# Kernel optimization log

Measured on AMD Instinct MI355X. Metric: run time of the kernel, lower is better.

Reference implementation:

```python
import jax, jax.numpy as jnp
import numpy as np

BEV_H, BEV_W, ED, HEADS, HD, LEVELS, POINTS, LAYERS = 200, 200, 128, 8, 16, 4, 8, 2
SPATIAL = [(128, 256), (64, 128), (32, 64), (16, 32)]
NV = sum(h * w for h, w in SPATIAL)
NQ = BEV_H * BEV_W
NCLS = 21


def setup_inputs() -> dict:
    key = jax.random.key(0)
    ks = iter(jax.random.split(key, 48))
    r = lambda shape, s=0.02: jax.random.normal(next(ks), shape, jnp.float32) * s
    inp = dict(
        value=r((1, NV, ED), 1.0),
        bev_queries=r((NQ, ED), 0.02),
        bev_pos=r((NQ, ED), 0.02),
        proj_indices=jax.random.randint(next(ks), (1, BEV_H, BEV_W), 0, 250000),
        Wv=r((LAYERS, ED, ED)), bv=jnp.zeros((LAYERS, ED)),
        Woff=r((LAYERS, ED, HEADS * LEVELS * POINTS * 2), 0.01),
        boff=jnp.zeros((LAYERS, HEADS * LEVELS * POINTS * 2)),
        Wattn=r((LAYERS, ED, HEADS * LEVELS * POINTS), 0.01),
        battn=jnp.zeros((LAYERS, HEADS * LEVELS * POINTS)),
        Wout=r((LAYERS, ED, ED)), bout=jnp.zeros((LAYERS, ED)),
        Wf1=r((LAYERS, ED, ED)), bf1=jnp.zeros((LAYERS, ED)),
        Wf2=r((LAYERS, ED, ED)), bf2=jnp.zeros((LAYERS, ED)),
        ln_g=jnp.ones((LAYERS, 2, ED)), ln_b=jnp.zeros((LAYERS, 2, ED)),
        cw1=r((128, ED, 7, 7), 0.01), g1=jnp.ones(128), b1=jnp.zeros(128),
        cw2=r((64, 128, 3, 3), 0.02), g2=jnp.ones(64), b2=jnp.zeros(64),
        cw3=r((48, 64, 3, 3), 0.02), g3=jnp.ones(48), b3=jnp.zeros(48),
        cw4=r((48, 48, 3, 3), 0.02), g4=jnp.ones(48), b4=jnp.zeros(48),
        objw=r((NCLS, 48, 1, 1), 0.05), objb=jnp.zeros(NCLS),
    )
    return inp


def _ln(x, g, b):
    m = x.mean(-1, keepdims=True)
    v = ((x - m) ** 2).mean(-1, keepdims=True)
    return (x - m) * jax.lax.rsqrt(v + 1e-5) * g + b


def _deform_attn(q, value, Wv, bv, Woff, boff, Wattn, battn, Wout, bout, ref):
    # multi-scale deformable attention (Deformable-DETR / BEVFormer core)
    v = (value[0] @ Wv + bv).reshape(NV, HEADS, HD)
    off = (q @ Woff + boff).reshape(NQ, HEADS, LEVELS, POINTS, 2)
    attn = jax.nn.softmax((q @ Wattn + battn).reshape(NQ, HEADS, LEVELS * POINTS), -1)
    attn = attn.reshape(NQ, HEADS, LEVELS, POINTS)
    out = jnp.zeros((HEADS, NQ, HD), jnp.float32)
    start = 0
    for l, (H, W) in enumerate(SPATIAL):
        vl = v[start:start + H * W].transpose(1, 0, 2)  # [HEADS, H*W, HD]
        start += H * W
        # normalized sampling locations in [0,1]
        loc = ref[:, None, None, :] + off[:, :, l] / jnp.array([W, H], jnp.float32)
        x = loc[..., 0] * W - 0.5  # grid_sample align_corners=False convention
        y = loc[..., 1] * H - 0.5  # [NQ, HEADS, POINTS]
        x0 = jnp.floor(x)
        y0 = jnp.floor(y)
        acc = jnp.zeros((HEADS, NQ, POINTS, HD), jnp.float32)
        for dx, dy in ((0, 0), (1, 0), (0, 1), (1, 1)):
            xc = x0 + dx
            yc = y0 + dy
            wgt = (1.0 - jnp.abs(x - xc)) * (1.0 - jnp.abs(y - yc))
            valid = (xc >= 0) & (xc < W) & (yc >= 0) & (yc < H)
            xi = jnp.clip(xc, 0, W - 1).astype(jnp.int32)
            yi = jnp.clip(yc, 0, H - 1).astype(jnp.int32)
            idx = (yi * W + xi).transpose(1, 0, 2)  # [HEADS, NQ, POINTS]
            g = jax.vmap(lambda vh, ih: vh[ih])(vl, idx)  # [HEADS, NQ, POINTS, HD]
            acc = acc + (wgt * valid).transpose(1, 0, 2)[..., None] * g
        out = out + jnp.einsum('nhp,hnpd->hnd', attn[:, :, l], acc)
    return out.transpose(1, 0, 2).reshape(NQ, ED) @ Wout + bout


def _bev_encoder(bev_queries, bev_pos, value, Wv, bv, Woff, boff, Wattn, battn, Wout, bout, Wf1, bf1, Wf2, bf2, ln_g, ln_b):
    gx = (jnp.arange(BEV_W, dtype=jnp.float32) + 0.5) / BEV_W
    gy = (jnp.arange(BEV_H, dtype=jnp.float32) + 0.5) / BEV_H
    ref = jnp.stack(jnp.meshgrid(gx, gy), -1).reshape(NQ, 2)  # (x, y)
    q = bev_queries
    for i in range(LAYERS):  # operation_order: cross_attn, norm, ffn, norm
        a = _deform_attn(q + bev_pos, value, Wv[i], bv[i], Woff[i], boff[i],
                         Wattn[i], battn[i], Wout[i], bout[i], ref)
        q = _ln(q + a, ln_g[i, 0], ln_b[i, 0])
        h = jax.nn.relu(q @ Wf1[i] + bf1[i]) @ Wf2[i] + bf2[i]
        q = _ln(q + h, ln_g[i, 1], ln_b[i, 1])
    return q


def _conv(x, w, p):
    return jax.lax.conv_general_dilated(x, w, (1, 1), [(p, p), (p, p)],
                                        dimension_numbers=('NCHW', 'OIHW', 'NCHW'))


def _bn_relu(x, g, b):
    m = x.mean((0, 2, 3), keepdims=True)
    v = x.var((0, 2, 3), keepdims=True)
    return jax.nn.relu((x - m) * jax.lax.rsqrt(v + 1e-5) * g[None, :, None, None] + b[None, :, None, None])


def reference(value, bev_queries, bev_pos, proj_indices, Wv, bv, Woff, boff, Wattn, battn, Wout, bout, Wf1, bf1, Wf2, bf2, ln_g, ln_b, cw1, g1, b1, cw2, g2, b2, cw3, g3, b3, cw4, g4, b4, objw, objb):
    observed_masks = proj_indices < jnp.max(proj_indices)  # mask_update
    q = _bev_encoder(bev_queries, bev_pos, value, Wv, bv, Woff, boff, Wattn, battn,
                     Wout, bout, Wf1, bf1, Wf2, bf2, ln_g, ln_b)
    mem = q.reshape(1, BEV_H, BEV_W, ED).transpose(0, 3, 1, 2)  # [1, ED, H, W]
    h = _bn_relu(_conv(mem, cw1, 3), g1, b1)
    h = _bn_relu(_conv(h, cw2, 1), g2, b2)
    h = _bn_relu(_conv(h, cw3, 1), g3, b3)
    h = _bn_relu(_conv(h, cw4, 1), g4, b4)
    semmap = _conv(h, objw, 0) + objb[None, :, None, None]
    return semmap, observed_masks
```

## Files before the change

kernel.cpp:

```cpp
#include <hip/hip_runtime.h>
#include <cstdint>
#include <cstddef>

#define NQ 40000
#define EDIM 128
#define NVAL 43520
#define NCLS 21

typedef unsigned short u16;
typedef unsigned int uint;
typedef short bf16x8 __attribute__((ext_vector_type(8)));
typedef float f32x4 __attribute__((ext_vector_type(4)));

__device__ inline u16 f2b(float f) {
    unsigned u = __float_as_uint(f);
    unsigned r = u + 0x7FFF + ((u >> 16) & 1);
    return (u16)(r >> 16);
}
__device__ inline float b2f(u16 v) {
    unsigned u = ((unsigned)v) << 16;
    return __uint_as_float(u);
}
__device__ inline float blo(uint u) { return __uint_as_float(u << 16); }
__device__ inline float bhi(uint u) { return __uint_as_float(u & 0xFFFF0000u); }

__global__ void reduce_max_int(const int* __restrict__ idx, int* __restrict__ mx) {
    int i = blockIdx.x * 256 + threadIdx.x;
    int v = (i < NQ) ? idx[i] : 0;
    for (int o = 32; o > 0; o >>= 1) v = max(v, __shfl_xor(v, o, 64));
    if ((threadIdx.x & 63) == 0) atomicMax(mx, v);
}

__global__ void write_mask(const int* __restrict__ idx, const int* __restrict__ mx,
                           float* __restrict__ out) {
    int i = blockIdx.x * 256 + threadIdx.x;
    if (i >= NQ) return;
    out[i] = (idx[i] < *mx) ? 1.0f : 0.0f;
}

__global__ void cvt_b_k(const float* __restrict__ src, u16* __restrict__ dst, int n8) {
    int i = blockIdx.x * 256 + threadIdx.x;
    if (i >= n8) return;
    const float4 a = ((const float4*)src)[i * 2];
    const float4 b = ((const float4*)src)[i * 2 + 1];
    u16 o[8] = {f2b(a.x), f2b(a.y), f2b(a.z), f2b(a.w), f2b(b.x), f2b(b.y), f2b(b.z), f2b(b.w)};
    ((uint4*)dst)[i] = *(const uint4*)o;
}

__global__ void add2b_k(const float* __restrict__ a, const float* __restrict__ b,
                        u16* __restrict__ c, int n8) {
    int i = blockIdx.x * 256 + threadIdx.x;
    if (i >= n8) return;
    const float4 a0 = ((const float4*)a)[i * 2], a1 = ((const float4*)a)[i * 2 + 1];
    const float4 b0 = ((const float4*)b)[i * 2], b1 = ((const float4*)b)[i * 2 + 1];
    u16 o[8] = {f2b(a0.x + b0.x), f2b(a0.y + b0.y), f2b(a0.z + b0.z), f2b(a0.w + b0.w),
                f2b(a1.x + b1.x), f2b(a1.y + b1.y), f2b(a1.z + b1.z), f2b(a1.w + b1.w)};
    ((uint4*)c)[i] = *(const uint4*)o;
}

__global__ void pack_enc_k(const float* __restrict__ Wv, const float* __restrict__ Woff,
                           const float* __restrict__ Wattn, const float* __restrict__ Wout,
                           const float* __restrict__ Wf1, const float* __restrict__ Wf2,
                           u16* __restrict__ dst) {
    int i = blockIdx.x * 256 + threadIdx.x;
    if (i >= 327680) return;
    int l = i / 163840, r = i % 163840;
    int k = r / 1280, col = r % 1280;
    const float* src; int N; int n; u16* d;
    u16* base = dst + (size_t)l * 163840;
    if (col < 128)       { src = Wv    + (size_t)l * 16384; N = 128; n = col;        d = base;          }
    else if (col < 640)  { src = Woff  + (size_t)l * 65536; N = 512; n = col - 128;  d = base + 16384;  }
    else if (col < 896)  { src = Wattn + (size_t)l * 32768; N = 256; n = col - 640;  d = base + 81920;  }
    else if (col < 1024) { src = Wout  + (size_t)l * 16384; N = 128; n = col - 896;  d = base + 114688; }
    else if (col < 1152) { src = Wf1   + (size_t)l * 16384; N = 128; n = col - 1024; d = base + 131072; }
    else                 { src = Wf2   + (size_t)l * 16384; N = 128; n = col - 1152; d = base + 147456; }
    d[(size_t)n * 128 + k] = f2b(src[(size_t)k * N + n]);
}

__global__ void pack_bias_k(const float* __restrict__ boff, const float* __restrict__ battn,
                            float* __restrict__ dst) {
    int i = blockIdx.x * 256 + threadIdx.x;
    if (i >= 1536) return;
    int l = i / 768, r = i % 768;
    dst[i] = (r < 512) ? boff[(size_t)l * 512 + r] : battn[(size_t)l * 256 + r - 512];
}

__global__ void pack_cw_k(const float* __restrict__ w, u16* __restrict__ wT,
                          int OC, int IC, int KS, int OCp, int ICp) {
    int i = blockIdx.x * 256 + threadIdx.x;
    int tot = KS * KS * OCp * ICp;
    if (i >= tot) return;
    int ic = i % ICp; int r = i / ICp;
    int oc = r % OCp; int tap = r / OCp;
    int ky = tap / KS, kx = tap % KS;
    float v = 0.f;
    if (oc < OC && ic < IC)
        v = w[(((size_t)oc * IC + ic) * KS + ky) * KS + kx];
    wT[i] = f2b(v);
}

__global__ __launch_bounds__(256) void gemm_mfma_k(
        const u16* __restrict__ A, const u16* __restrict__ BT,
        const float* __restrict__ bias, float* __restrict__ Cf,
        u16* __restrict__ Cb, int N, int relu) {
    __shared__ u16 As[64 * 136];
    __shared__ u16 Bs[64 * 136];
    const int m0 = blockIdx.x * 64, n0 = blockIdx.y * 64;
    const int t = threadIdx.x;
#pragma unroll
    for (int ci = t; ci < 1024; ci += 256) {
        int r = ci >> 4, c = ci & 15;
        *(uint4*)&As[r * 136 + c * 8] = *(const uint4*)&A[(size_t)(m0 + r) * 128 + c * 8];
        *(uint4*)&Bs[r * 136 + c * 8] = *(const uint4*)&BT[(size_t)(n0 + r) * 128 + c * 8];
    }
    __syncthreads();
    const int wave = t >> 6, lane = t & 63;
    const int wm = (wave & 1) * 32, wn = (wave >> 1) * 32;
    const int lr = lane & 15, lk = (lane >> 4) * 8;
    f32x4 acc[2][2] = {};
#pragma unroll
    for (int ks = 0; ks < 4; ks++) {
        bf16x8 a0 = *(const bf16x8*)&As[(wm + lr) * 136 + ks * 32 + lk];
        bf16x8 a1 = *(const bf16x8*)&As[(wm + 16 + lr) * 136 + ks * 32 + lk];
        bf16x8 b0 = *(const bf16x8*)&Bs[(wn + lr) * 136 + ks * 32 + lk];
        bf16x8 b1 = *(const bf16x8*)&Bs[(wn + 16 + lr) * 136 + ks * 32 + lk];
        acc[0][0] = __builtin_amdgcn_mfma_f32_16x16x32_bf16(a0, b0, acc[0][0], 0, 0, 0);
        acc[0][1] = __builtin_amdgcn_mfma_f32_16x16x32_bf16(a0, b1, acc[0][1], 0, 0, 0);
        acc[1][0] = __builtin_amdgcn_mfma_f32_16x16x32_bf16(a1, b0, acc[1][0], 0, 0, 0);
        acc[1][1] = __builtin_amdgcn_mfma_f32_16x16x32_bf16(a1, b1, acc[1][1], 0, 0, 0);
    }
    float bj0 = bias[n0 + wn + lr];
    float bj1 = bias[n0 + wn + 16 + lr];
#pragma unroll
    for (int i = 0; i < 2; i++) {
#pragma unroll
        for (int j = 0; j < 2; j++) {
            float bb = j ? bj1 : bj0;
#pragma unroll
            for (int r = 0; r < 4; r++) {
                int ml = wm + i * 16 + (lane >> 4) * 4 + r;
                int nl = wn + j * 16 + lr;
                float v = acc[i][j][r] + bb;
                if (relu) v = fmaxf(v, 0.f);
                size_t o = (size_t)(m0 + ml) * N + n0 + nl;
                if (Cf) Cf[o] = v;
                if (Cb) Cb[o] = f2b(v);
            }
        }
    }
}

template <int KS, int ICP>
__global__ __launch_bounds__(256) void conv3_mfma_k(
        const u16* __restrict__ pimg, const u16* __restrict__ wT,
        float* __restrict__ out, int OCtot) {
    constexpr int PAD = KS / 2;
    constexpr int WIN = 64 + KS - 1;
    constexpr int LDSTR = ICP + 8;
    constexpr int KSTEPS = ICP / 32;
    constexpr int CHUNKS = 2 * WIN * (ICP / 8);
    __shared__ u16 As[2 * WIN * LDSTR];
    const int bx = blockIdx.x;
    const int y = (bx >> 2) * 2;
    const int xc = bx & 3;
    const int x0 = (xc == 3) ? 136 : xc * 64;
    const int n0 = blockIdx.y * 64;
    const int t = threadIdx.x;
    const int wave = t >> 6, lane = t & 63;
    const int rowsel = wave >> 1;
    const int wn = (wave & 1) * 32;
    const int lr = lane & 15, lkq = lane >> 4, lk = lkq * 8;
    f32x4 acc[4][2] = {};
    bf16x8 bbA[2][KSTEPS], bbB[2][KSTEPS];

    auto loadB = [&](int tap, bf16x8 (&bb)[2][KSTEPS]) {
        const u16* wb = wT + ((size_t)tap * OCtot + n0) * ICP;
#pragma unroll
        for (int ks = 0; ks < KSTEPS; ks++) {
            bb[0][ks] = *(const bf16x8*)&wb[(size_t)(wn + lr) * ICP + ks * 32 + lk];
            bb[1][ks] = *(const bf16x8*)&wb[(size_t)(wn + 16 + lr) * ICP + ks * 32 + lk];
        }
    };

    for (int ky = 0; ky < KS; ky++) {
        __syncthreads();
        for (int ci = t; ci < CHUNKS; ci += 256) {
            int w2 = ci / (WIN * (ICP / 8));
            int rem = ci - w2 * WIN * (ICP / 8);
            int r = rem / (ICP / 8), c = rem - r * (ICP / 8);
            const u16* src = pimg +
                (((size_t)(y + w2 + ky + 3 - PAD)) * 208 + (x0 + 3 - PAD)) * ICP;
            *(uint4*)&As[(w2 * WIN + r) * LDSTR + c * 8] = *(const uint4*)&src[(size_t)r * ICP + c * 8];
        }
        __syncthreads();
        loadB(ky * KS, bbA);
        const u16* asb = &As[rowsel * WIN * LDSTR];
#pragma unroll
        for (int kx = 0; kx < KS; kx++) {
            if (kx + 1 < KS) {
                if (kx & 1) loadB(ky * KS + kx + 1, bbA);
                else        loadB(ky * KS + kx + 1, bbB);
            }
#pragma unroll
            for (int ks = 0; ks < KSTEPS; ks++) {
                bf16x8 a0 = *(const bf16x8*)&asb[(lr + kx) * LDSTR + ks * 32 + lk];
                bf16x8 a1 = *(const bf16x8*)&asb[(lr + 16 + kx) * LDSTR + ks * 32 + lk];
                bf16x8 a2 = *(const bf16x8*)&asb[(lr + 32 + kx) * LDSTR + ks * 32 + lk];
                bf16x8 a3 = *(const bf16x8*)&asb[(lr + 48 + kx) * LDSTR + ks * 32 + lk];
#pragma unroll
                for (int j = 0; j < 2; j++) {
                    bf16x8 bj = (kx & 1) ? bbB[j][ks] : bbA[j][ks];
                    acc[0][j] = __builtin_amdgcn_mfma_f32_16x16x32_bf16(a0, bj, acc[0][j], 0, 0, 0);
                    acc[1][j] = __builtin_amdgcn_mfma_f32_16x16x32_bf16(a1, bj, acc[1][j], 0, 0, 0);
                    acc[2][j] = __builtin_amdgcn_mfma_f32_16x16x32_bf16(a2, bj, acc[2][j], 0, 0, 0);
                    acc[3][j] = __builtin_amdgcn_mfma_f32_16x16x32_bf16(a3, bj, acc[3][j], 0, 0, 0);
                }
            }
        }
    }
    const int px0 = (y + rowsel) * 200 + x0;
#pragma unroll
    for (int i = 0; i < 4; i++) {
#pragma unroll
        for (int j = 0; j < 2; j++) {
#pragma unroll
            for (int r = 0; r < 4; r++) {
                int ml = i * 16 + lkq * 4 + r;
                int nl = wn + j * 16 + lr;
                out[(size_t)(px0 + ml) * OCtot + n0 + nl] = acc[i][j][r];
            }
        }
    }
}

__global__ __launch_bounds__(256) void deform2_k(
        const u16* __restrict__ v, const u16* __restrict__ oa,
        u16* __restrict__ outb, int q0, int nq) {
    const int t = threadIdx.x;
    const int wq = t >> 6;
    const int lane = t & 63;
    const int h = lane >> 3;
    const int cl = lane & 7;
    const int qi = blockIdx.x * 4 + wq;
    if (qi >= nq) return;
    const int gq = q0 + qi;
    const float rx = ((gq % 200) + 0.5f) / 200.f;
    const float ry = ((gq / 200) + 0.5f) / 200.f;

    const uint* lp = (const uint*)(oa + (size_t)qi * 768 + 512 + h * 32);
    uint lw[16];
#pragma unroll
    for (int i = 0; i < 16; i++) lw[i] = lp[i];
    float lg[32];
#pragma unroll
    for (int i = 0; i < 16; i++) { lg[2 * i] = blo(lw[i]); lg[2 * i + 1] = bhi(lw[i]); }
    float mx = -1e30f;
#pragma unroll
    for (int i = 0; i < 32; i++) mx = fmaxf(mx, lg[i]);
    float ssum = 0.f;
#pragma unroll
    for (int i = 0; i < 32; i++) { lg[i] = __expf(lg[i] - mx); ssum += lg[i]; }
    const float inv = 1.f / ssum;

    const uint* op = (const uint*)(oa + (size_t)qi * 768 + h * 64);

    const int HS[4] = {128, 64, 32, 16};
    const int WS[4] = {256, 128, 64, 32};
    const int ST[4] = {0, 32768, 40960, 43008};
    float acc0 = 0.f, acc1 = 0.f;
#pragma unroll
    for (int l = 0; l < 4; l++) {
        const int H = HS[l], W = WS[l];
        const float fW = (float)W, fH = (float)H;
        const u16* vb = v + (size_t)ST[l] * 128 + h * 16 + cl * 2;
#pragma unroll
        for (int p = 0; p < 8; p++) {
            uint pr = op[l * 8 + p];
            float ox = blo(pr), oy = bhi(pr);
            float xx = rx * fW + ox - 0.5f;
            float yy = ry * fH + oy - 0.5f;
            float xf = floorf(xx), yf = floorf(yy);
            int ix = (int)xf, iy = (int)yf;
            float fx = xx - xf, fy = yy - yf;
            float aw = lg[l * 8 + p] * inv;
            int x1 = ix + 1, y1 = iy + 1;
            bool vx0 = (unsigned)ix < (unsigned)W;
            bool vx1 = (unsigned)x1 < (unsigned)W;
            bool vy0 = (unsigned)iy < (unsigned)H;
            bool vy1 = (unsigned)y1 < (unsigned)H;
            int cx0 = min(max(ix, 0), W - 1), cx1 = min(max(x1, 0), W - 1);
            int cy0 = min(max(iy, 0), H - 1), cy1 = min(max(y1, 0), H - 1);
            float w00 = (vx0 && vy0) ? (1.f - fx) * (1.f - fy) * aw : 0.f;
            float w10 = (vx1 && vy0) ? fx * (1.f - fy) * aw : 0.f;
            float w01 = (vx0 && vy1) ? (1.f - fx) * fy * aw : 0.f;
            float w11 = (vx1 && vy1) ? fx * fy * aw : 0.f;
            uint u00 = *(const uint*)(vb + (size_t)(cy0 * W + cx0) * 128);
            uint u10 = *(const uint*)(vb + (size_t)(cy0 * W + cx1) * 128);
            uint u01 = *(const uint*)(vb + (size_t)(cy1 * W + cx0) * 128);
            uint u11 = *(const uint*)(vb + (size_t)(cy1 * W + cx1) * 128);
            acc0 = fmaf(w00, blo(u00), acc0); acc1 = fmaf(w00, bhi(u00), acc1);
            acc0 = fmaf(w10, blo(u10), acc0); acc1 = fmaf(w10, bhi(u10), acc1);
            acc0 = fmaf(w01, blo(u01), acc0); acc1 = fmaf(w01, bhi(u01), acc1);
            acc0 = fmaf(w11, blo(u11), acc0); acc1 = fmaf(w11, bhi(u11), acc1);
        }
    }
    uint o = (uint)f2b(acc0) | ((uint)f2b(acc1) << 16);
    *(uint*)(outb + (size_t)gq * 128 + h * 16 + cl * 2) = o;
}

__global__ __launch_bounds__(256) void add_ln_k(
        float* __restrict__ q, const float* __restrict__ a,
        const float* __restrict__ g, const float* __restrict__ b,
        u16* __restrict__ qb) {
    const int row = blockIdx.x * 4 + (threadIdx.x >> 6);
    const int lane = threadIdx.x & 63;
    float s0 = q[(size_t)row * 128 + lane] + a[(size_t)row * 128 + lane];
    float s1 = q[(size_t)row * 128 + 64 + lane] + a[(size_t)row * 128 + 64 + lane];
    float sum = s0 + s1;
    for (int o = 32; o > 0; o >>= 1) sum += __shfl_xor(sum, o, 64);
    float mean = sum * (1.f / 128.f);
    float d0 = s0 - mean, d1 = s1 - mean;
    float vs = d0 * d0 + d1 * d1;
    for (int o = 32; o > 0; o >>= 1) vs += __shfl_xor(vs, o, 64);
    float inv = rsqrtf(vs * (1.f / 128.f) + 1e-5f);
    float o0 = d0 * inv * g[lane] + b[lane];
    float o1 = d1 * inv * g[64 + lane] + b[64 + lane];
    q[(size_t)row * 128 + lane] = o0;
    q[(size_t)row * 128 + 64 + lane] = o1;
    qb[(size_t)row * 128 + lane] = f2b(o0);
    qb[(size_t)row * 128 + 64 + lane] = f2b(o1);
}

__global__ void fill_pimg_k(const u16* __restrict__ qb, u16* __restrict__ pimg) {
    int i = blockIdx.x * 256 + threadIdx.x;
    if (i >= 640000) return;
    int p = i >> 4, c8 = i & 15;
    int y = p / 200, x = p - y * 200;
    ((uint4*)pimg)[((size_t)(y + 3) * 208 + (x + 3)) * 16 + c8] = ((const uint4*)qb)[i];
}

__global__ __launch_bounds__(256) void bn_stats2_k(const float* __restrict__ x,
                                                   float* __restrict__ acc,
                                                   int cSh, int ppb) {
    const int t = threadIdx.x;
    const int Cp = 1 << cSh;
    const int c = t & (Cp - 1);
    const int sub = t >> cSh;
    const int nsub = 256 >> cSh;
    float s = 0.f, s2 = 0.f;
    const int pbase = blockIdx.x * ppb;
    for (int i = sub; i < ppb; i += nsub) {
        float v = x[(size_t)(pbase + i) * Cp + c];
        s += v; s2 += v * v;
    }
    __shared__ float ls[256], ls2[256];
    ls[t] = s; ls2[t] = s2;
    __syncthreads();
    if (t < Cp) {
        for (int k = 1; k < nsub; k++) { s += ls[t + k * Cp]; s2 += ls2[t + k * Cp]; }
        atomicAdd(&acc[2 * t], s);
        atomicAdd(&acc[2 * t + 1], s2);
    }
}

__global__ void bn_fin_k(const float* __restrict__ acc, float* __restrict__ mv, int C) {
    int t = threadIdx.x;
    if (t >= C) return;
    float m = acc[2 * t] * (1.f / 40000.f);
    float var = acc[2 * t + 1] * (1.f / 40000.f) - m * m;
    mv[2 * t] = m;
    mv[2 * t + 1] = rsqrtf(var + 1e-5f);
}

__global__ void bn_apply_pad_k(const float* __restrict__ x, const float* __restrict__ mv,
                               const float* __restrict__ g, const float* __restrict__ b,
                               u16* __restrict__ outp, int cSh, int Creal) {
    int i = blockIdx.x * 256 + threadIdx.x;
    int Cp = 1 << cSh;
    if (i >= 40000 * Cp) return;
    int c = i & (Cp - 1);
    int p = i >> cSh;
    int y = p / 200, x_ = p - y * 200;
    float v = 0.f;
    if (c < Creal) v = fmaxf((x[i] - mv[2 * c]) * mv[2 * c + 1] * g[c] + b[c], 0.f);
    outp[((size_t)(y + 3) * 208 + (x_ + 3)) * Cp + c] = f2b(v);
}

__global__ void bn_apply2_k(const float* __restrict__ x, const float* __restrict__ mv,
                            const float* __restrict__ g, const float* __restrict__ b,
                            u16* __restrict__ outb, int cSh, int Creal) {
    int i = blockIdx.x * 256 + threadIdx.x;
    int Cp = 1 << cSh;
    if (i >= 40000 * Cp) return;
    int c = i & (Cp - 1);
    float v = 0.f;
    if (c < Creal) v = fmaxf((x[i] - mv[2 * c]) * mv[2 * c + 1] * g[c] + b[c], 0.f);
    outb[i] = f2b(v);
}

__global__ void obj_conv_k(const u16* __restrict__ in, const float* __restrict__ w,
                           const float* __restrict__ bias, float* __restrict__ out) {
    int p = blockIdx.x * 256 + threadIdx.x;
    if (p >= 40000) return;
    float xin[48];
#pragma unroll
    for (int c = 0; c < 48; c++) xin[c] = b2f(in[(size_t)p * 64 + c]);
    for (int o = 0; o < NCLS; o++) {
        float acc = bias[o];
#pragma unroll
        for (int c = 0; c < 48; c++) acc += xin[c] * w[o * 48 + c];
        out[(size_t)o * 40000 + p] = acc;
    }
}

extern "C" void kernel_launch(void* const* d_in, const int* in_sizes, int n_in,
                              void* d_out, int out_size, void* d_ws, size_t ws_size,
                              hipStream_t stream) {
    const float* value   = (const float*)d_in[0];
    const float* bev_q   = (const float*)d_in[1];
    const float* bev_pos = (const float*)d_in[2];
    const int*   proj    = (const int*)d_in[3];
    const float* Wv      = (const float*)d_in[4];
    const float* bv      = (const float*)d_in[5];
    const float* Woff    = (const float*)d_in[6];
    const float* boff    = (const float*)d_in[7];
    const float* Wattn   = (const float*)d_in[8];
    const float* battn   = (const float*)d_in[9];
    const float* Wout    = (const float*)d_in[10];
    const float* bout    = (const float*)d_in[11];
    const float* Wf1     = (const float*)d_in[12];
    const float* bf1     = (const float*)d_in[13];
    const float* Wf2     = (const float*)d_in[14];
    const float* bf2     = (const float*)d_in[15];
    const float* ln_g    = (const float*)d_in[16];
    const float* ln_b    = (const float*)d_in[17];
    const float* cw1     = (const float*)d_in[18];
    const float* g1      = (const float*)d_in[19];
    const float* b1      = (const float*)d_in[20];
    const float* cw2     = (const float*)d_in[21];
    const float* g2      = (const float*)d_in[22];
    const float* b2      = (const float*)d_in[23];
    const float* cw3     = (const float*)d_in[24];
    const float* g3      = (const float*)d_in[25];
    const float* b3      = (const float*)d_in[26];
    const float* cw4     = (const float*)d_in[27];
    const float* g4      = (const float*)d_in[28];
    const float* b4      = (const float*)d_in[29];
    const float* objw    = (const float*)d_in[30];
    const float* objb    = (const float*)d_in[31];
    float* out = (float*)d_out;

    float* WSb = (float*)d_ws;
    float* q     = WSb + 0;
    u16*   qb    = (u16*)(WSb + 5120000);
    u16*   qpb   = (u16*)(WSb + 7680000);
    u16*   valb  = (u16*)(WSb + 10240000);
    u16*   vbufb = (u16*)(WSb + 13025280);
    u16*   fb    = (u16*)(WSb + 15810560);
    float* tmp   = WSb + 18882560;
    u16*   aob   = (u16*)(WSb + 24002560);
    u16*   hb    = (u16*)(WSb + 26562560);
    u16*   wenc  = (u16*)(WSb + 29122560);
    u16*   wcv   = (u16*)(WSb + 29286400);
    float* bnacc = WSb + 29761536;
    float* bnmv  = WSb + 29762048;
    int*   maxi  = (int*)(WSb + 29762304);
    float* fbias = WSb + 29762308;

    u16*   pimg = (u16*)(WSb + 10240000);
    float* c1f  = tmp;
    u16*   c1b  = (u16*)(WSb + 13025280);
    float* c2f  = WSb + 0;
    u16*   c2b  = (u16*)(WSb + 5120000);
    float* c3f  = WSb + 2560000;
    u16*   c3b  = (u16*)(WSb + 7680000);
    float* c4f  = WSb + 0;
    u16*   c4b  = (u16*)(WSb + 15810560);

    const size_t L = 163840;
    u16* WvT[2]; u16* WoffT[2]; u16* WoutT[2]; u16* Wf1T[2]; u16* Wf2T[2];
    for (int l = 0; l < 2; l++) {
        u16* base = wenc + l * L;
        WvT[l]    = base;
        WoffT[l]  = base + 16384;
        WoutT[l]  = base + 114688;
        Wf1T[l]   = base + 131072;
        Wf2T[l]   = base + 147456;
    }
    u16* w1T = wcv;
    u16* w2T = wcv + 802816;
    u16* w3T = wcv + 876544;
    u16* w4T = wcv + 913408;

    hipMemsetAsync(maxi, 0, sizeof(int), stream);
    reduce_max_int<<<157, 256, 0, stream>>>(proj, maxi);
    write_mask<<<157, 256, 0, stream>>>(proj, maxi, out + 840000);

    pack_enc_k<<<1280, 256, 0, stream>>>(Wv, Woff, Wattn, Wout, Wf1, Wf2, wenc);
    pack_bias_k<<<6, 256, 0, stream>>>(boff, battn, fbias);
    pack_cw_k<<<3136, 256, 0, stream>>>(cw1, w1T, 128, 128, 7, 128, 128);
    pack_cw_k<<<288, 256, 0, stream>>>(cw2, w2T, 64, 128, 3, 64, 128);
    pack_cw_k<<<144, 256, 0, stream>>>(cw3, w3T, 48, 64, 3, 64, 64);
    pack_cw_k<<<144, 256, 0, stream>>>(cw4, w4T, 48, 48, 3, 64, 64);
    cvt_b_k<<<2720, 256, 0, stream>>>(value, valb, NVAL * 128 / 8);

    hipMemcpyAsync(q, bev_q, (size_t)NQ * EDIM * sizeof(float),
                   hipMemcpyDeviceToDevice, stream);
    const int CH0 = 19968, CH1 = 20032;
    for (int l = 0; l < 2; l++) {
        gemm_mfma_k<<<dim3(680, 2), 256, 0, stream>>>(
            valb, WvT[l], bv + (size_t)l * 128, nullptr, vbufb, 128, 0);
        add2b_k<<<2500, 256, 0, stream>>>(q, bev_pos, qpb, NQ * 128 / 8);
        for (int cidx = 0; cidx < 2; cidx++) {
            int qs = cidx ? CH0 : 0;
            int nq = cidx ? CH1 : CH0;
            gemm_mfma_k<<<dim3(nq / 64, 12), 256, 0, stream>>>(
                qpb + (size_t)qs * 128, WoffT[l], fbias + (size_t)l * 768,
                nullptr, fb, 768, 0);
            deform2_k<<<nq / 4, 256, 0, stream>>>(vbufb, fb, aob, qs, nq);
        }
        gemm_mfma_k<<<dim3(625, 2), 256, 0, stream>>>(
            aob, WoutT[l], bout + (size_t)l * 128, tmp, nullptr, 128, 0);
        add_ln_k<<<10000, 256, 0, stream>>>(q, tmp, ln_g + (size_t)(l * 2 + 0) * 128,
                                            ln_b + (size_t)(l * 2 + 0) * 128, qb);
        gemm_mfma_k<<<dim3(625, 2), 256, 0, stream>>>(
            qb, Wf1T[l], bf1 + (size_t)l * 128, nullptr, hb, 128, 1);
        gemm_mfma_k<<<dim3(625, 2), 256, 0, stream>>>(
            hb, Wf2T[l], bf2 + (size_t)l * 128, tmp, nullptr, 128, 0);
        add_ln_k<<<10000, 256, 0, stream>>>(q, tmp, ln_g + (size_t)(l * 2 + 1) * 128,
                                            ln_b + (size_t)(l * 2 + 1) * 128, qb);
    }

    hipMemsetAsync(pimg, 0, (size_t)206 * 208 * 128 * 2, stream);
    fill_pimg_k<<<2500, 256, 0, stream>>>(qb, pimg);

    conv3_mfma_k<7, 128><<<dim3(400, 2), 256, 0, stream>>>(pimg, w1T, c1f, 128);
    hipMemsetAsync(bnacc, 0, 512 * sizeof(float), stream);
    bn_stats2_k<<<125, 256, 0, stream>>>(c1f, bnacc, 7, 320);
    bn_fin_k<<<1, 128, 0, stream>>>(bnacc, bnmv, 128);
    hipMemsetAsync(c1b, 0, (size_t)206 * 208 * 128 * 2, stream);
    bn_apply_pad_k<<<20000, 256, 0, stream>>>(c1f, bnmv, g1, b1, c1b, 7, 128);

    conv3_mfma_k<3, 128><<<dim3(400, 1), 256, 0, stream>>>(c1b, w2T, c2f, 64);
    hipMemsetAsync(bnacc, 0, 512 * sizeof(float), stream);
    bn_stats2_k<<<125, 256, 0, stream>>>(c2f, bnacc, 6, 320);
    bn_fin_k<<<1, 64, 0, stream>>>(bnacc, bnmv, 64);
    hipMemsetAsync(c2b, 0, (size_t)206 * 208 * 64 * 2, stream);
    bn_apply_pad_k<<<10000, 256, 0, stream>>>(c2f, bnmv, g2, b2, c2b, 6, 64);

    conv3_mfma_k<3, 64><<<dim3(400, 1), 256, 0, stream>>>(c2b, w3T, c3f, 64);
    hipMemsetAsync(bnacc, 0, 512 * sizeof(float), stream);
    bn_stats2_k<<<125, 256, 0, stream>>>(c3f, bnacc, 6, 320);
    bn_fin_k<<<1, 48, 0, stream>>>(bnacc, bnmv, 48);
    hipMemsetAsync(c3b, 0, (size_t)206 * 208 * 64 * 2, stream);
    bn_apply_pad_k<<<10000, 256, 0, stream>>>(c3f, bnmv, g3, b3, c3b, 6, 48);

    conv3_mfma_k<3, 64><<<dim3(400, 1), 256, 0, stream>>>(c3b, w4T, c4f, 64);
    hipMemsetAsync(bnacc, 0, 512 * sizeof(float), stream);
    bn_stats2_k<<<125, 256, 0, stream>>>(c4f, bnacc, 6, 320);
    bn_fin_k<<<1, 48, 0, stream>>>(bnacc, bnmv, 48);
    bn_apply2_k<<<10000, 256, 0, stream>>>(c4f, bnmv, g4, b4, c4b, 6, 48);

    obj_conv_k<<<157, 256, 0, stream>>>(c4b, objw, objb, out);
}
```

Measured before the change: 1.141 ms.

## Retile conv to one row per block, widen deform loads, fuse padding into fills

The conv kernel now computes one output row per block, with a 2x2 wave split over pixels and output channels. It stages a single input row window in LDS and double-buffers the weight registers across taps, which doubles the grid and shrinks LDS use. The deformable attention kernel now handles two queries per wave and loads 4 channels per lane with 64-bit gathers. The padded image fill and the BN apply kernels write the zero border themselves, removing separate memsets. The trade-off is less reuse of weights across rows in the conv and more blocks overall.

```diff
diff --git a/kernel.cpp b/kernel.cpp
--- a/kernel.cpp
+++ b/kernel.cpp
@@ -151,81 +151,75 @@
 }
 
 template <int KS, int ICP>
-__global__ __launch_bounds__(256) void conv3_mfma_k(
+__global__ __launch_bounds__(256) void conv4_mfma_k(
         const u16* __restrict__ pimg, const u16* __restrict__ wT,
         float* __restrict__ out, int OCtot) {
     constexpr int PAD = KS / 2;
     constexpr int WIN = 64 + KS - 1;
     constexpr int LDSTR = ICP + 8;
     constexpr int KSTEPS = ICP / 32;
-    constexpr int CHUNKS = 2 * WIN * (ICP / 8);
-    __shared__ u16 As[2 * WIN * LDSTR];
+    constexpr int NTAP = KS * KS;
+    __shared__ u16 As[WIN * LDSTR];
     const int bx = blockIdx.x;
-    const int y = (bx >> 2) * 2;
+    const int y = bx >> 2;
     const int xc = bx & 3;
     const int x0 = (xc == 3) ? 136 : xc * 64;
     const int n0 = blockIdx.y * 64;
     const int t = threadIdx.x;
     const int wave = t >> 6, lane = t & 63;
-    const int rowsel = wave >> 1;
-    const int wn = (wave & 1) * 32;
+    const int wm = (wave & 1) * 32, wn = (wave >> 1) * 32;
     const int lr = lane & 15, lkq = lane >> 4, lk = lkq * 8;
-    f32x4 acc[4][2] = {};
-    bf16x8 bbA[2][KSTEPS], bbB[2][KSTEPS];
-
-    auto loadB = [&](int tap, bf16x8 (&bb)[2][KSTEPS]) {
-        const u16* wb = wT + ((size_t)tap * OCtot + n0) * ICP;
-#pragma unroll
-        for (int ks = 0; ks < KSTEPS; ks++) {
-            bb[0][ks] = *(const bf16x8*)&wb[(size_t)(wn + lr) * ICP + ks * 32 + lk];
-            bb[1][ks] = *(const bf16x8*)&wb[(size_t)(wn + 16 + lr) * ICP + ks * 32 + lk];
-        }
-    };
+
+    f32x4 acc[2][2] = {};
+    const u16* wbase = wT + (size_t)n0 * ICP;
+
+    bf16x8 cur0[KSTEPS], cur1[KSTEPS], nxt0[KSTEPS], nxt1[KSTEPS];
+#pragma unroll
+    for (int ks = 0; ks < KSTEPS; ks++) {
+        cur0[ks] = *(const bf16x8*)&wbase[(size_t)(wn + lr) * ICP + ks * 32 + lk];
+        cur1[ks] = *(const bf16x8*)&wbase[(size_t)(wn + 16 + lr) * ICP + ks * 32 + lk];
+    }
 
     for (int ky = 0; ky < KS; ky++) {
         __syncthreads();
-        for (int ci = t; ci < CHUNKS; ci += 256) {
-            int w2 = ci / (WIN * (ICP / 8));
-            int rem = ci - w2 * WIN * (ICP / 8);
-            int r = rem / (ICP / 8), c = rem - r * (ICP / 8);
-            const u16* src = pimg +
-                (((size_t)(y + w2 + ky + 3 - PAD)) * 208 + (x0 + 3 - PAD)) * ICP;
-            *(uint4*)&As[(w2 * WIN + r) * LDSTR + c * 8] = *(const uint4*)&src[(size_t)r * ICP + c * 8];
+        const u16* src = pimg + (((size_t)(y + ky + 3 - PAD)) * 208 + (x0 + 3 - PAD)) * ICP;
+        for (int ci = t; ci < WIN * (ICP / 8); ci += 256) {
+            int r = ci / (ICP / 8), c = ci - r * (ICP / 8);
+            *(uint4*)&As[r * LDSTR + c * 8] = *(const uint4*)&src[(size_t)r * ICP + c * 8];
         }
         __syncthreads();
-        loadB(ky * KS, bbA);
-        const u16* asb = &As[rowsel * WIN * LDSTR];
 #pragma unroll
         for (int kx = 0; kx < KS; kx++) {
-            if (kx + 1 < KS) {
-                if (kx & 1) loadB(ky * KS + kx + 1, bbA);
-                else        loadB(ky * KS + kx + 1, bbB);
-            }
-#pragma unroll
-            for (int ks = 0; ks < KSTEPS; ks++) {
-                bf16x8 a0 = *(const bf16x8*)&asb[(lr + kx) * LDSTR + ks * 32 + lk];
-                bf16x8 a1 = *(const bf16x8*)&asb[(lr + 16 + kx) * LDSTR + ks * 32 + lk];
-                bf16x8 a2 = *(const bf16x8*)&asb[(lr + 32 + kx) * LDSTR + ks * 32 + lk];
-                bf16x8 a3 = *(const bf16x8*)&asb[(lr + 48 + kx) * LDSTR + ks * 32 + lk];
-#pragma unroll
-                for (int j = 0; j < 2; j++) {
-                    bf16x8 bj = (kx & 1) ? bbB[j][ks] : bbA[j][ks];
-                    acc[0][j] = __builtin_amdgcn_mfma_f32_16x16x32_bf16(a0, bj, acc[0][j], 0, 0, 0);
-                    acc[1][j] = __builtin_amdgcn_mfma_f32_16x16x32_bf16(a1, bj, acc[1][j], 0, 0, 0);
-                    acc[2][j] = __builtin_amdgcn_mfma_f32_16x16x32_bf16(a2, bj, acc[2][j], 0, 0, 0);
-                    acc[3][j] = __builtin_amdgcn_mfma_f32_16x16x32_bf16(a3, bj, acc[3][j], 0, 0, 0);
+            const int tap = ky * KS + kx;
+            if (tap + 1 < NTAP) {
+                const u16* wb = wbase + (size_t)(tap + 1) * OCtot * ICP;
+#pragma unroll
+                for (int ks = 0; ks < KSTEPS; ks++) {
+                    nxt0[ks] = *(const bf16x8*)&wb[(size_t)(wn + lr) * ICP + ks * 32 + lk];
+                    nxt1[ks] = *(const bf16x8*)&wb[(size_t)(wn + 16 + lr) * ICP + ks * 32 + lk];
                 }
             }
+#pragma unroll
+            for (int ks = 0; ks < KSTEPS; ks++) {
+                bf16x8 a0 = *(const bf16x8*)&As[(wm + lr + kx) * LDSTR + ks * 32 + lk];
+                bf16x8 a1 = *(const bf16x8*)&As[(wm + 16 + lr + kx) * LDSTR + ks * 32 + lk];
+                acc[0][0] = __builtin_amdgcn_mfma_f32_16x16x32_bf16(a0, cur0[ks], acc[0][0], 0, 0, 0);
+                acc[0][1] = __builtin_amdgcn_mfma_f32_16x16x32_bf16(a0, cur1[ks], acc[0][1], 0, 0, 0);
+                acc[1][0] = __builtin_amdgcn_mfma_f32_16x16x32_bf16(a1, cur0[ks], acc[1][0], 0, 0, 0);
+                acc[1][1] = __builtin_amdgcn_mfma_f32_16x16x32_bf16(a1, cur1[ks], acc[1][1], 0, 0, 0);
+            }
+#pragma unroll
+            for (int ks = 0; ks < KSTEPS; ks++) { cur0[ks] = nxt0[ks]; cur1[ks] = nxt1[ks]; }
         }
     }
-    const int px0 = (y + rowsel) * 200 + x0;
-#pragma unroll
-    for (int i = 0; i < 4; i++) {
+    const int px0 = y * 200 + x0;
+#pragma unroll
+    for (int i = 0; i < 2; i++) {
 #pragma unroll
         for (int j = 0; j < 2; j++) {
 #pragma unroll
             for (int r = 0; r < 4; r++) {
-                int ml = i * 16 + lkq * 4 + r;
+                int ml = wm + i * 16 + lkq * 4 + r;
                 int nl = wn + j * 16 + lr;
                 out[(size_t)(px0 + ml) * OCtot + n0 + nl] = acc[i][j][r];
             }
@@ -233,27 +227,26 @@
     }
 }
 
-__global__ __launch_bounds__(256) void deform2_k(
+__global__ __launch_bounds__(256) void deform3_k(
         const u16* __restrict__ v, const u16* __restrict__ oa,
         u16* __restrict__ outb, int q0, int nq) {
     const int t = threadIdx.x;
     const int wq = t >> 6;
     const int lane = t & 63;
-    const int h = lane >> 3;
-    const int cl = lane & 7;
-    const int qi = blockIdx.x * 4 + wq;
+    const int s = lane >> 5;
+    const int l32 = lane & 31;
+    const int h = l32 >> 2;
+    const int cl = l32 & 3;
+    const int qi = blockIdx.x * 8 + wq * 2 + s;
     if (qi >= nq) return;
     const int gq = q0 + qi;
     const float rx = ((gq % 200) + 0.5f) / 200.f;
     const float ry = ((gq / 200) + 0.5f) / 200.f;
 
     const uint* lp = (const uint*)(oa + (size_t)qi * 768 + 512 + h * 32);
-    uint lw[16];
-#pragma unroll
-    for (int i = 0; i < 16; i++) lw[i] = lp[i];
     float lg[32];
 #pragma unroll
-    for (int i = 0; i < 16; i++) { lg[2 * i] = blo(lw[i]); lg[2 * i + 1] = bhi(lw[i]); }
+    for (int i = 0; i < 16; i++) { uint u = lp[i]; lg[2 * i] = blo(u); lg[2 * i + 1] = bhi(u); }
     float mx = -1e30f;
 #pragma unroll
     for (int i = 0; i < 32; i++) mx = fmaxf(mx, lg[i]);
@@ -267,12 +260,12 @@
     const int HS[4] = {128, 64, 32, 16};
     const int WS[4] = {256, 128, 64, 32};
     const int ST[4] = {0, 32768, 40960, 43008};
-    float acc0 = 0.f, acc1 = 0.f;
+    float a0 = 0.f, a1 = 0.f, a2 = 0.f, a3 = 0.f;
 #pragma unroll
     for (int l = 0; l < 4; l++) {
         const int H = HS[l], W = WS[l];
         const float fW = (float)W, fH = (float)H;
-        const u16* vb = v + (size_t)ST[l] * 128 + h * 16 + cl * 2;
+        const u16* vb = v + (size_t)ST[l] * 128 + h * 16 + cl * 4;
 #pragma unroll
         for (int p = 0; p < 8; p++) {
             uint pr = op[l * 8 + p];
@@ -294,18 +287,24 @@
             float w10 = (vx1 && vy0) ? fx * (1.f - fy) * aw : 0.f;
             float w01 = (vx0 && vy1) ? (1.f - fx) * fy * aw : 0.f;
             float w11 = (vx1 && vy1) ? fx * fy * aw : 0.f;
-            uint u00 = *(const uint*)(vb + (size_t)(cy0 * W + cx0) * 128);
-            uint u10 = *(const uint*)(vb + (size_t)(cy0 * W + cx1) * 128);
-            uint u01 = *(const uint*)(vb + (size_t)(cy1 * W + cx0) * 128);
-            uint u11 = *(const uint*)(vb + (size_t)(cy1 * W + cx1) * 128);
-            acc0 = fmaf(w00, blo(u00), acc0); acc1 = fmaf(w00, bhi(u00), acc1);
-            acc0 = fmaf(w10, blo(u10), acc0); acc1 = fmaf(w10, bhi(u10), acc1);
-            acc0 = fmaf(w01, blo(u01), acc0); acc1 = fmaf(w01, bhi(u01), acc1);
-            acc0 = fmaf(w11, blo(u11), acc0); acc1 = fmaf(w11, bhi(u11), acc1);
+            uint2 u00 = *(const uint2*)(vb + (size_t)(cy0 * W + cx0) * 128);
+            uint2 u10 = *(const uint2*)(vb + (size_t)(cy0 * W + cx1) * 128);
+            uint2 u01 = *(const uint2*)(vb + (size_t)(cy1 * W + cx0) * 128);
+            uint2 u11 = *(const uint2*)(vb + (size_t)(cy1 * W + cx1) * 128);
+            a0 = fmaf(w00, blo(u00.x), a0); a1 = fmaf(w00, bhi(u00.x), a1);
+            a2 = fmaf(w00, blo(u00.y), a2); a3 = fmaf(w00, bhi(u00.y), a3);
+            a0 = fmaf(w10, blo(u10.x), a0); a1 = fmaf(w10, bhi(u10.x), a1);
+            a2 = fmaf(w10, blo(u10.y), a2); a3 = fmaf(w10, bhi(u10.y), a3);
+            a0 = fmaf(w01, blo(u01.x), a0); a1 = fmaf(w01, bhi(u01.x), a1);
+            a2 = fmaf(w01, blo(u01.y), a2); a3 = fmaf(w01, bhi(u01.y), a3);
+            a0 = fmaf(w11, blo(u11.x), a0); a1 = fmaf(w11, bhi(u11.x), a1);
+            a2 = fmaf(w11, blo(u11.y), a2); a3 = fmaf(w11, bhi(u11.y), a3);
         }
     }
-    uint o = (uint)f2b(acc0) | ((uint)f2b(acc1) << 16);
-    *(uint*)(outb + (size_t)gq * 128 + h * 16 + cl * 2) = o;
+    uint2 o;
+    o.x = (uint)f2b(a0) | ((uint)f2b(a1) << 16);
+    o.y = (uint)f2b(a2) | ((uint)f2b(a3) << 16);
+    *(uint2*)(outb + (size_t)gq * 128 + h * 16 + cl * 4) = o;
 }
 
 __global__ __launch_bounds__(256) void add_ln_k(
@@ -331,12 +330,15 @@
     qb[(size_t)row * 128 + 64 + lane] = f2b(o1);
 }
 
-__global__ void fill_pimg_k(const u16* __restrict__ qb, u16* __restrict__ pimg) {
-    int i = blockIdx.x * 256 + threadIdx.x;
-    if (i >= 640000) return;
-    int p = i >> 4, c8 = i & 15;
-    int y = p / 200, x = p - y * 200;
-    ((uint4*)pimg)[((size_t)(y + 3) * 208 + (x + 3)) * 16 + c8] = ((const uint4*)qb)[i];
+__global__ void fill_pimg2_k(const u16* __restrict__ qb, u16* __restrict__ pimg) {
+    int i = blockIdx.x * 256 + threadIdx.x;
+    if (i >= 685568) return;
+    int pp = i >> 4, c8 = i & 15;
+    int py = pp / 208, px = pp - py * 208;
+    uint4 val = {0u, 0u, 0u, 0u};
+    if (py >= 3 && py < 203 && px >= 3 && px < 203)
+        val = ((const uint4*)qb)[((size_t)((py - 3) * 200 + (px - 3))) * 16 + c8];
+    ((uint4*)pimg)[i] = val;
 }
 
 __global__ __launch_bounds__(256) void bn_stats2_k(const float* __restrict__ x,
@@ -372,18 +374,21 @@
     mv[2 * t + 1] = rsqrtf(var + 1e-5f);
 }
 
-__global__ void bn_apply_pad_k(const float* __restrict__ x, const float* __restrict__ mv,
-                               const float* __restrict__ g, const float* __restrict__ b,
-                               u16* __restrict__ outp, int cSh, int Creal) {
+__global__ void bn_apply_pad2_k(const float* __restrict__ x, const float* __restrict__ mv,
+                                const float* __restrict__ g, const float* __restrict__ b,
+                                u16* __restrict__ outp, int cSh, int Creal) {
     int i = blockIdx.x * 256 + threadIdx.x;
     int Cp = 1 << cSh;
-    if (i >= 40000 * Cp) return;
+    if (i >= 206 * 208 * Cp) return;
     int c = i & (Cp - 1);
-    int p = i >> cSh;
-    int y = p / 200, x_ = p - y * 200;
+    int pp = i >> cSh;
+    int py = pp / 208, px = pp - py * 208;
     float v = 0.f;
-    if (c < Creal) v = fmaxf((x[i] - mv[2 * c]) * mv[2 * c + 1] * g[c] + b[c], 0.f);
-    outp[((size_t)(y + 3) * 208 + (x_ + 3)) * Cp + c] = f2b(v);
+    if (c < Creal && py >= 3 && py < 203 && px >= 3 && px < 203) {
+        int p = (py - 3) * 200 + (px - 3);
+        v = fmaxf((x[(size_t)p * Cp + c] - mv[2 * c]) * mv[2 * c + 1] * g[c] + b[c], 0.f);
+    }
+    outp[i] = f2b(v);
 }
 
 __global__ void bn_apply2_k(const float* __restrict__ x, const float* __restrict__ mv,
@@ -517,7 +522,7 @@
             gemm_mfma_k<<<dim3(nq / 64, 12), 256, 0, stream>>>(
                 qpb + (size_t)qs * 128, WoffT[l], fbias + (size_t)l * 768,
                 nullptr, fb, 768, 0);
-            deform2_k<<<nq / 4, 256, 0, stream>>>(vbufb, fb, aob, qs, nq);
+            deform3_k<<<nq / 8, 256, 0, stream>>>(vbufb, fb, aob, qs, nq);
         }
         gemm_mfma_k<<<dim3(625, 2), 256, 0, stream>>>(
             aob, WoutT[l], bout + (size_t)l * 128, tmp, nullptr, 128, 0);
@@ -531,31 +536,27 @@
                                             ln_b + (size_t)(l * 2 + 1) * 128, qb);
     }
 
-    hipMemsetAsync(pimg, 0, (size_t)206 * 208 * 128 * 2, stream);
-    fill_pimg_k<<<2500, 256, 0, stream>>>(qb, pimg);
-
-    conv3_mfma_k<7, 128><<<dim3(400, 2), 256, 0, stream>>>(pimg, w1T, c1f, 128);
+    fill_pimg2_k<<<2678, 256, 0, stream>>>(qb, pimg);
+
+    conv4_mfma_k<7, 128><<<dim3(800, 2), 256, 0, stream>>>(pimg, w1T, c1f, 128);
     hipMemsetAsync(bnacc, 0, 512 * sizeof(float), stream);
     bn_stats2_k<<<125, 256, 0, stream>>>(c1f, bnacc, 7, 320);
     bn_fin_k<<<1, 128, 0, stream>>>(bnacc, bnmv, 128);
-    hipMemsetAsync(c1b, 0, (size_t)206 * 208 * 128 * 2, stream);
-    bn_apply_pad_k<<<20000, 256, 0, stream>>>(c1f, bnmv, g1, b1, c1b, 7, 128);
-
-    conv3_mfma_k<3, 128><<<dim3(400, 1), 256, 0, stream>>>(c1b, w2T, c2f, 64);
+    bn_apply_pad2_k<<<21424, 256, 0, stream>>>(c1f, bnmv, g1, b1, c1b, 7, 128);
+
+    conv4_mfma_k<3, 128><<<dim3(800, 1), 256, 0, stream>>>(c1b, w2T, c2f, 64);
     hipMemsetAsync(bnacc, 0, 512 * sizeof(float), stream);
     bn_stats2_k<<<125, 256, 0, stream>>>(c2f, bnacc, 6, 320);
     bn_fin_k<<<1, 64, 0, stream>>>(bnacc, bnmv, 64);
-    hipMemsetAsync(c2b, 0, (size_t)206 * 208 * 64 * 2, stream);
-    bn_apply_pad_k<<<10000, 256, 0, stream>>>(c2f, bnmv, g2, b2, c2b, 6, 64);
-
-    conv3_mfma_k<3, 64><<<dim3(400, 1), 256, 0, stream>>>(c2b, w3T, c3f, 64);
+    bn_apply_pad2_k<<<10712, 256, 0, stream>>>(c2f, bnmv, g2, b2, c2b, 6, 64);
+
+    conv4_mfma_k<3, 64><<<dim3(800, 1), 256, 0, stream>>>(c2b, w3T, c3f, 64);
     hipMemsetAsync(bnacc, 0, 512 * sizeof(float), stream);
     bn_stats2_k<<<125, 256, 0, stream>>>(c3f, bnacc, 6, 320);
     bn_fin_k<<<1, 48, 0, stream>>>(bnacc, bnmv, 48);
-    hipMemsetAsync(c3b, 0, (size_t)206 * 208 * 64 * 2, stream);
-    bn_apply_pad_k<<<10000, 256, 0, stream>>>(c3f, bnmv, g3, b3, c3b, 6, 48);
-
-    conv3_mfma_k<3, 64><<<dim3(400, 1), 256, 0, stream>>>(c3b, w4T, c4f, 64);
+    bn_apply_pad2_k<<<10712, 256, 0, stream>>>(c3f, bnmv, g3, b3, c3b, 6, 48);
+
+    conv4_mfma_k<3, 64><<<dim3(800, 1), 256, 0, stream>>>(c3b, w4T, c4f, 64);
     hipMemsetAsync(bnacc, 0, 512 * sizeof(float), stream);
     bn_stats2_k<<<125, 256, 0, stream>>>(c4f, bnacc, 6, 320);
     bn_fin_k<<<1, 48, 0, stream>>>(bnacc, bnmv, 48);
```

After: 1.161 ms. Within noise of the previous version (+1.7%).
